# Performance work log

Hardware: AMD Instinct MI355X
Metric: run time of the kernel (lower is better)

The kernel has to match this reference:

```python
import jax, jax.numpy as jnp
import numpy as np

N_ATOMS, N_NBH, N_IN, N_FILTERS, N_OUT, N_GAUSS = 10000, 48, 128, 128, 128, 25
R_CUTOFF = 5.0
LOG2 = float(np.log(2.0))


def ssp(v):
    # shifted softplus, the SchNet activation
    return jax.nn.softplus(v) - LOG2


def setup_inputs() -> dict:
    key = jax.random.key(0)
    ks = jax.random.split(key, 10)
    x = jax.random.normal(ks[0], (N_ATOMS, N_IN), dtype=jnp.float32)
    dR = jax.random.uniform(ks[1], (N_ATOMS, N_NBH), dtype=jnp.float32) * 10.0  # distances in [0,10)
    dR_expanded = jax.random.normal(ks[2], (N_ATOMS, N_NBH, N_GAUSS), dtype=jnp.float32)
    pairwise_mask = jnp.ones((N_ATOMS, N_NBH), dtype=jnp.float32)
    neighbors_idx = jax.random.randint(ks[3], (N_ATOMS, N_NBH), 0, N_ATOMS, dtype=jnp.int32)
    s = 1.0 / np.sqrt(N_FILTERS)
    W1 = jax.random.normal(ks[4], (N_GAUSS, N_FILTERS), dtype=jnp.float32) * (1.0 / np.sqrt(N_GAUSS))
    b1 = jnp.zeros((N_FILTERS,), dtype=jnp.float32)
    W2 = jax.random.normal(ks[5], (N_FILTERS, N_FILTERS), dtype=jnp.float32) * s
    b2 = jnp.zeros((N_FILTERS,), dtype=jnp.float32)
    W_in2f = jax.random.normal(ks[6], (N_IN, N_FILTERS), dtype=jnp.float32) * (1.0 / np.sqrt(N_IN))
    W_f2out = jax.random.normal(ks[7], (N_FILTERS, N_OUT), dtype=jnp.float32) * s
    b_f2out = jnp.zeros((N_OUT,), dtype=jnp.float32)
    return {"x": x, "dR": dR, "dR_expanded": dR_expanded, "pairwise_mask": pairwise_mask,
            "neighbors_idx": neighbors_idx, "W1": W1, "b1": b1, "W2": W2, "b2": b2,
            "W_in2f": W_in2f, "W_f2out": W_f2out, "b_f2out": b_f2out}


def reference(x, dR, dR_expanded, pairwise_mask, neighbors_idx,
              W1, b1, W2, b2, W_in2f, W_f2out, b_f2out):
    # FilterNetwork: Dense + ssp + Dense, on Gaussian-smeared distances -> [N, K, F]
    W = jnp.einsum('nkg,gf->nkf', dR_expanded, W1) + b1
    W = jnp.einsum('nkf,fh->nkh', ssp(W), W2) + b2
    # HardCutoff: 1 where within cutoff
    C = (dR <= R_CUTOFF).astype(W.dtype)           # [N, K]
    W = W * C[..., None]
    # in2f (no bias), gather neighbor features
    y = x @ W_in2f                                  # [N, F]
    y = jnp.take(y, neighbors_idx, axis=0)          # [N, K, F] (gather == take_along_axis path)
    # filter-weighted multiply + masked sum aggregation over neighbor axis
    y = y * W
    y = jnp.sum(y * pairwise_mask[..., None], axis=1)  # [N, F]
    # f2out: Linear + shifted softplus
    return ssp(y @ W_f2out + b_f2out)               # [N, n_out]
```

## Files before the change

### kernel.cpp

```cpp
#include <hip/hip_runtime.h>
#include <hip/hip_bf16.h>


#define NA 10000
#define NK 48
#define NF 128
#define HP  136
#define YFP 136

typedef __bf16 bf16x8 __attribute__((ext_vector_type(8)));
typedef float  f32x4  __attribute__((ext_vector_type(4)));

__device__ __forceinline__ unsigned short f2bs(float x) {
    return __builtin_bit_cast(unsigned short, (__bf16)x);
}
__device__ __forceinline__ float bs2f(unsigned short u) {
    return (float)__builtin_bit_cast(__bf16, u);
}
__device__ __forceinline__ float sspf(float v) {
    return fmaxf(v, 0.0f) + __logf(1.0f + __expf(-fabsf(v))) - 0.69314718056f;
}

__global__ __launch_bounds__(256) void prep_weights(
    const float* __restrict__ W1,
    const float* __restrict__ W2,
    const float* __restrict__ Wi,
    const float* __restrict__ Wo,
    unsigned short* __restrict__ wsb)
{
    int i = blockIdx.x * 256 + threadIdx.x;
    if (i < 4096) {
        int f = i >> 5, g = i & 31;
        wsb[i] = (g < 25) ? f2bs(W1[g * NF + f]) : (unsigned short)0;
    } else if (i < 20480) {
        int j = i - 4096; int h = j >> 7, k = j & 127;
        wsb[i] = f2bs(W2[k * NF + h]);
    } else if (i < 36864) {
        int j = i - 20480; int f = j >> 7, k = j & 127;
        wsb[i] = f2bs(Wi[k * NF + f]);
    } else if (i < 53248) {
        int j = i - 36864; int f = j >> 7, k = j & 127;
        wsb[i] = f2bs(Wo[k * NF + f]);
    }
}

__global__ __launch_bounds__(256) void in2f_mfma(
    const float* __restrict__ x,
    const unsigned short* __restrict__ WiT,
    unsigned short* __restrict__ yfeatb)
{
    const int tid = threadIdx.x;
    const int w = tid >> 6;
    const int lane = tid & 63;
    const int r = lane & 15;
    const int q = lane >> 4;
    const int m0 = blockIdx.x * 64 + w * 16;
    const int row = m0 + r;
    const bool rv = (row < NA);

    f32x4 acc[8];
    #pragma unroll
    for (int nt = 0; nt < 8; ++nt) { acc[nt][0]=0.f; acc[nt][1]=0.f; acc[nt][2]=0.f; acc[nt][3]=0.f; }

    #pragma unroll
    for (int ks = 0; ks < 4; ++ks) {
        bf16x8 a;
        if (rv) {
            const float4* xp = (const float4*)(x + (size_t)row * NF + ks * 32 + q * 8);
            float4 v0 = xp[0], v1 = xp[1];
            a[0]=(__bf16)v0.x; a[1]=(__bf16)v0.y; a[2]=(__bf16)v0.z; a[3]=(__bf16)v0.w;
            a[4]=(__bf16)v1.x; a[5]=(__bf16)v1.y; a[6]=(__bf16)v1.z; a[7]=(__bf16)v1.w;
        } else {
            #pragma unroll
            for (int j = 0; j < 8; ++j) a[j] = (__bf16)0.0f;
        }
        #pragma unroll
        for (int nt = 0; nt < 8; ++nt) {
            bf16x8 b = *(const bf16x8*)(WiT + (nt * 16 + r) * NF + ks * 32 + q * 8);
            acc[nt] = __builtin_amdgcn_mfma_f32_16x16x32_bf16(a, b, acc[nt], 0, 0, 0);
        }
    }
    #pragma unroll
    for (int nt = 0; nt < 8; ++nt) {
        #pragma unroll
        for (int reg = 0; reg < 4; ++reg) {
            int orow = m0 + q * 4 + reg;
            if (orow < NA)
                yfeatb[(size_t)orow * NF + nt * 16 + r] = f2bs(acc[nt][reg]);
        }
    }
}

__global__ __launch_bounds__(256) void cfconv_mfma(
    const float* __restrict__ dR,
    const float* __restrict__ dRe,
    const float* __restrict__ mask,
    const int*   __restrict__ nbr,
    const float* __restrict__ b1,
    const float* __restrict__ b2,
    const unsigned short* __restrict__ W1T,
    const unsigned short* __restrict__ W2T,
    const unsigned short* __restrict__ yfeatb,
    float* __restrict__ yout)
{
    __shared__ __align__(16) unsigned short s_H[NK * HP];
    __shared__ __align__(16) unsigned short s_yf[NK * YFP];
    __shared__ float s_cm[NK];

    const int tid = threadIdx.x;
    const int n = blockIdx.x;
    const int w = tid >> 6;
    const int lane = tid & 63;
    const int r = lane & 15;
    const int q = lane >> 4;
    const int nt0 = w * 2;

    const int kb = tid >> 4;
    const int sp = tid & 15;
    const int nb0 = nbr[n * NK + kb] * NF;
    const int nb1 = nbr[n * NK + kb + 16] * NF;
    const int nb2 = nbr[n * NK + kb + 32] * NF;
    bf16x8 g0 = *(const bf16x8*)(yfeatb + nb0 + sp * 8);
    bf16x8 g1 = *(const bf16x8*)(yfeatb + nb1 + sp * 8);
    bf16x8 g2 = *(const bf16x8*)(yfeatb + nb2 + sp * 8);

    bf16x8 bfr0 = *(const bf16x8*)(W1T + ((nt0    ) * 16 + r) * 32 + q * 8);
    bf16x8 bfr1 = *(const bf16x8*)(W1T + ((nt0 + 1) * 16 + r) * 32 + q * 8);
    bf16x8 bw[2][4];
    #pragma unroll
    for (int t = 0; t < 2; ++t)
        #pragma unroll
        for (int ks = 0; ks < 4; ++ks)
            bw[t][ks] = *(const bf16x8*)(W2T + ((nt0 + t) * 16 + r) * NF + ks * 32 + q * 8);

    if (tid < NK) {
        float d = dR[n * NK + tid];
        float m = mask[n * NK + tid];
        s_cm[tid] = (d <= 5.0f) ? m : 0.0f;
    }

    const float bias1a = b1[nt0 * 16 + r];
    const float bias1b = b1[nt0 * 16 + 16 + r];
    const float bias2a = b2[nt0 * 16 + r];
    const float bias2b = b2[nt0 * 16 + 16 + r];

    const float* dre_n = dRe + (size_t)n * (NK * 25);
    #pragma unroll
    for (int mt = 0; mt < 3; ++mt) {
        bf16x8 a;
        if (q < 3) {
            float av[8];
            __builtin_memcpy(av, dre_n + (mt * 16 + r) * 25 + q * 8, 32);
            #pragma unroll
            for (int j = 0; j < 8; ++j) a[j] = (__bf16)av[j];
        } else {
            float v = dre_n[(mt * 16 + r) * 25 + 24];
            a[0] = (__bf16)v;
            #pragma unroll
            for (int j = 1; j < 8; ++j) a[j] = (__bf16)0.0f;
        }
        f32x4 zf; zf[0]=0.f; zf[1]=0.f; zf[2]=0.f; zf[3]=0.f;
        f32x4 h0v = __builtin_amdgcn_mfma_f32_16x16x32_bf16(a, bfr0, zf, 0, 0, 0);
        f32x4 h1v = __builtin_amdgcn_mfma_f32_16x16x32_bf16(a, bfr1, zf, 0, 0, 0);
        #pragma unroll
        for (int reg = 0; reg < 4; ++reg) {
            int k = mt * 16 + q * 4 + reg;
            s_H[k * HP + nt0 * 16 + r]      = f2bs(sspf(h0v[reg] + bias1a));
            s_H[k * HP + nt0 * 16 + 16 + r] = f2bs(sspf(h1v[reg] + bias1b));
        }
    }

    *(bf16x8*)(&s_yf[(kb     ) * YFP + sp * 8]) = g0;
    *(bf16x8*)(&s_yf[(kb + 16) * YFP + sp * 8]) = g1;
    *(bf16x8*)(&s_yf[(kb + 32) * YFP + sp * 8]) = g2;

    __syncthreads();

    f32x4 acc[3][2];
    #pragma unroll
    for (int mt = 0; mt < 3; ++mt)
        #pragma unroll
        for (int t = 0; t < 2; ++t) { acc[mt][t][0]=0.f; acc[mt][t][1]=0.f; acc[mt][t][2]=0.f; acc[mt][t][3]=0.f; }

    #pragma unroll
    for (int ks = 0; ks < 4; ++ks) {
        #pragma unroll
        for (int mt = 0; mt < 3; ++mt) {
            bf16x8 a = *(const bf16x8*)(&s_H[(mt * 16 + r) * HP + ks * 32 + q * 8]);
            acc[mt][0] = __builtin_amdgcn_mfma_f32_16x16x32_bf16(a, bw[0][ks], acc[mt][0], 0, 0, 0);
            acc[mt][1] = __builtin_amdgcn_mfma_f32_16x16x32_bf16(a, bw[1][ks], acc[mt][1], 0, 0, 0);
        }
    }

    float part0 = 0.f, part1 = 0.f;
    const int h0 = nt0 * 16 + r;
    #pragma unroll
    for (int mt = 0; mt < 3; ++mt) {
        #pragma unroll
        for (int reg = 0; reg < 4; ++reg) {
            int k = mt * 16 + q * 4 + reg;
            float cmk = s_cm[k];
            part0 += cmk * (acc[mt][0][reg] + bias2a) * bs2f(s_yf[k * YFP + h0]);
            part1 += cmk * (acc[mt][1][reg] + bias2b) * bs2f(s_yf[k * YFP + h0 + 16]);
        }
    }
    part0 += __shfl_xor(part0, 16);
    part0 += __shfl_xor(part0, 32);
    part1 += __shfl_xor(part1, 16);
    part1 += __shfl_xor(part1, 32);
    if (q == 0) {
        yout[(size_t)n * NF + h0]      = part0;
        yout[(size_t)n * NF + h0 + 16] = part1;
    }
}

__global__ __launch_bounds__(256) void f2out_mfma(
    const unsigned short* __restrict__ WoT,
    const float* __restrict__ bo,
    float* io)
{
    const int tid = threadIdx.x;
    const int w = tid >> 6;
    const int lane = tid & 63;
    const int r = lane & 15;
    const int q = lane >> 4;
    const int m0 = blockIdx.x * 64 + w * 16;
    const int row = m0 + r;
    const bool rv = (row < NA);

    f32x4 acc[8];
    #pragma unroll
    for (int nt = 0; nt < 8; ++nt) { acc[nt][0]=0.f; acc[nt][1]=0.f; acc[nt][2]=0.f; acc[nt][3]=0.f; }

    #pragma unroll
    for (int ks = 0; ks < 4; ++ks) {
        bf16x8 a;
        if (rv) {
            const float4* yp = (const float4*)(io + (size_t)row * NF + ks * 32 + q * 8);
            float4 v0 = yp[0], v1 = yp[1];
            a[0]=(__bf16)v0.x; a[1]=(__bf16)v0.y; a[2]=(__bf16)v0.z; a[3]=(__bf16)v0.w;
            a[4]=(__bf16)v1.x; a[5]=(__bf16)v1.y; a[6]=(__bf16)v1.z; a[7]=(__bf16)v1.w;
        } else {
            #pragma unroll
            for (int j = 0; j < 8; ++j) a[j] = (__bf16)0.0f;
        }
        #pragma unroll
        for (int nt = 0; nt < 8; ++nt) {
            bf16x8 b = *(const bf16x8*)(WoT + (nt * 16 + r) * NF + ks * 32 + q * 8);
            acc[nt] = __builtin_amdgcn_mfma_f32_16x16x32_bf16(a, b, acc[nt], 0, 0, 0);
        }
    }
    #pragma unroll
    for (int nt = 0; nt < 8; ++nt) {
        float bia = bo[nt * 16 + r];
        #pragma unroll
        for (int reg = 0; reg < 4; ++reg) {
            int orow = m0 + q * 4 + reg;
            if (orow < NA)
                io[(size_t)orow * NF + nt * 16 + r] = sspf(acc[nt][reg] + bia);
        }
    }
}

extern "C" void kernel_launch(void* const* d_in, const int* in_sizes, int n_in,
                              void* d_out, int out_size, void* d_ws, size_t ws_size,
                              hipStream_t stream)
{
    const float* x    = (const float*)d_in[0];
    const float* dR   = (const float*)d_in[1];
    const float* dRe  = (const float*)d_in[2];
    const float* mask = (const float*)d_in[3];
    const int*   nbr  = (const int*)d_in[4];
    const float* W1   = (const float*)d_in[5];
    const float* b1   = (const float*)d_in[6];
    const float* W2   = (const float*)d_in[7];
    const float* b2   = (const float*)d_in[8];
    const float* Wi2f = (const float*)d_in[9];
    const float* Wf2o = (const float*)d_in[10];
    const float* bf2o = (const float*)d_in[11];
    float* out = (float*)d_out;

    unsigned short* wsb = (unsigned short*)d_ws;
    unsigned short* W1T    = wsb;
    unsigned short* W2T    = wsb + 4096;
    unsigned short* WiT    = wsb + 20480;
    unsigned short* WoT    = wsb + 36864;
    unsigned short* yfeatb = wsb + 53248;

    prep_weights<<<208, 256, 0, stream>>>(W1, W2, Wi2f, Wf2o, wsb);
    in2f_mfma<<<157, 256, 0, stream>>>(x, WiT, yfeatb);
    cfconv_mfma<<<NA, 256, 0, stream>>>(dR, dRe, mask, nbr, b1, b2,
                                        W1T, W2T, yfeatb, out);
    f2out_mfma<<<157, 256, 0, stream>>>(WoT, bf2o, out);
}
```

Measured before the change: 198.4 us.

## Fuse f2out into cfconv and merge weight prep into in2f kernel

Merges the weight-prep and in2f kernels into one launch: extra blocks convert W1/W2/Wo to bf16, while the in2f blocks transpose Wi into shared memory themselves. The f2out linear plus shifted softplus is fused into the per-atom cfconv kernel, so each atom's aggregated features stay in shared memory and never make a round trip through global memory. The filter MFMA operands are swapped so the neighbor reduction becomes shuffles inside a 16-lane group. In exchange, each cfconv block runs a 1-row MFMA that wastes most of its 16 rows, and it adds a second barrier.

```diff
diff --git a/kernel.cpp b/kernel.cpp
--- a/kernel.cpp
+++ b/kernel.cpp
@@ -21,35 +21,49 @@
     return fmaxf(v, 0.0f) + __logf(1.0f + __expf(-fabsf(v))) - 0.69314718056f;
 }
 
-__global__ __launch_bounds__(256) void prep_weights(
+__global__ __launch_bounds__(256) void in2f_prep(
+    const float* __restrict__ x,
+    const float* __restrict__ Wi,
     const float* __restrict__ W1,
     const float* __restrict__ W2,
-    const float* __restrict__ Wi,
     const float* __restrict__ Wo,
-    unsigned short* __restrict__ wsb)
-{
-    int i = blockIdx.x * 256 + threadIdx.x;
-    if (i < 4096) {
-        int f = i >> 5, g = i & 31;
-        wsb[i] = (g < 25) ? f2bs(W1[g * NF + f]) : (unsigned short)0;
-    } else if (i < 20480) {
-        int j = i - 4096; int h = j >> 7, k = j & 127;
-        wsb[i] = f2bs(W2[k * NF + h]);
-    } else if (i < 36864) {
-        int j = i - 20480; int f = j >> 7, k = j & 127;
-        wsb[i] = f2bs(Wi[k * NF + f]);
-    } else if (i < 53248) {
-        int j = i - 36864; int f = j >> 7, k = j & 127;
-        wsb[i] = f2bs(Wo[k * NF + f]);
-    }
-}
-
-__global__ __launch_bounds__(256) void in2f_mfma(
-    const float* __restrict__ x,
-    const unsigned short* __restrict__ WiT,
+    unsigned short* __restrict__ wsb,
     unsigned short* __restrict__ yfeatb)
 {
     const int tid = threadIdx.x;
+
+    if (blockIdx.x >= 157) {
+        int i = (blockIdx.x - 157) * 256 + tid;
+        if (i < 4096) {
+            int f = i >> 5, g = i & 31;
+            wsb[i] = (g < 25) ? f2bs(W1[g * NF + f]) : (unsigned short)0;
+        } else if (i < 20480) {
+            int j = i - 4096; int h = j >> 7, k = j & 127;
+            wsb[i] = f2bs(W2[k * NF + h]);
+        } else {
+            int j = i - 20480; int f = j >> 7, k = j & 127;
+            wsb[i] = f2bs(Wo[k * NF + f]);
+        }
+        return;
+    }
+
+    __shared__ __align__(16) unsigned short s_wi[NF * 136];
+    {
+        const float4* wi4 = (const float4*)Wi;
+        #pragma unroll
+        for (int it = 0; it < 16; ++it) {
+            int idx4 = it * 256 + tid;
+            float4 v = wi4[idx4];
+            int i = idx4 >> 5;
+            int f = (idx4 & 31) * 4;
+            s_wi[(f + 0) * 136 + i] = f2bs(v.x);
+            s_wi[(f + 1) * 136 + i] = f2bs(v.y);
+            s_wi[(f + 2) * 136 + i] = f2bs(v.z);
+            s_wi[(f + 3) * 136 + i] = f2bs(v.w);
+        }
+    }
+    __syncthreads();
+
     const int w = tid >> 6;
     const int lane = tid & 63;
     const int r = lane & 15;
@@ -76,7 +90,7 @@
         }
         #pragma unroll
         for (int nt = 0; nt < 8; ++nt) {
-            bf16x8 b = *(const bf16x8*)(WiT + (nt * 16 + r) * NF + ks * 32 + q * 8);
+            bf16x8 b = *(const bf16x8*)(&s_wi[(nt * 16 + r) * 136 + ks * 32 + q * 8]);
             acc[nt] = __builtin_amdgcn_mfma_f32_16x16x32_bf16(a, b, acc[nt], 0, 0, 0);
         }
     }
@@ -98,13 +112,16 @@
     const int*   __restrict__ nbr,
     const float* __restrict__ b1,
     const float* __restrict__ b2,
+    const float* __restrict__ bf2o,
     const unsigned short* __restrict__ W1T,
     const unsigned short* __restrict__ W2T,
+    const unsigned short* __restrict__ WoT,
     const unsigned short* __restrict__ yfeatb,
-    float* __restrict__ yout)
+    float* __restrict__ out)
 {
     __shared__ __align__(16) unsigned short s_H[NK * HP];
     __shared__ __align__(16) unsigned short s_yf[NK * YFP];
+    __shared__ __align__(16) float s_y[NF];
     __shared__ float s_cm[NK];
 
     const int tid = threadIdx.x;
@@ -141,8 +158,6 @@
 
     const float bias1a = b1[nt0 * 16 + r];
     const float bias1b = b1[nt0 * 16 + 16 + r];
-    const float bias2a = b2[nt0 * 16 + r];
-    const float bias2b = b2[nt0 * 16 + 16 + r];
 
     const float* dre_n = dRe + (size_t)n * (NK * 25);
     #pragma unroll
@@ -176,88 +191,85 @@
 
     __syncthreads();
 
-    f32x4 acc[3][2];
-    #pragma unroll
-    for (int mt = 0; mt < 3; ++mt)
-        #pragma unroll
-        for (int t = 0; t < 2; ++t) { acc[mt][t][0]=0.f; acc[mt][t][1]=0.f; acc[mt][t][2]=0.f; acc[mt][t][3]=0.f; }
+    f32x4 acc[2][3];
+    #pragma unroll
+    for (int t = 0; t < 2; ++t)
+        #pragma unroll
+        for (int kt = 0; kt < 3; ++kt) { acc[t][kt][0]=0.f; acc[t][kt][1]=0.f; acc[t][kt][2]=0.f; acc[t][kt][3]=0.f; }
 
     #pragma unroll
     for (int ks = 0; ks < 4; ++ks) {
         #pragma unroll
-        for (int mt = 0; mt < 3; ++mt) {
-            bf16x8 a = *(const bf16x8*)(&s_H[(mt * 16 + r) * HP + ks * 32 + q * 8]);
-            acc[mt][0] = __builtin_amdgcn_mfma_f32_16x16x32_bf16(a, bw[0][ks], acc[mt][0], 0, 0, 0);
-            acc[mt][1] = __builtin_amdgcn_mfma_f32_16x16x32_bf16(a, bw[1][ks], acc[mt][1], 0, 0, 0);
-        }
-    }
-
-    float part0 = 0.f, part1 = 0.f;
-    const int h0 = nt0 * 16 + r;
-    #pragma unroll
-    for (int mt = 0; mt < 3; ++mt) {
+        for (int kt = 0; kt < 3; ++kt) {
+            bf16x8 bh = *(const bf16x8*)(&s_H[(kt * 16 + r) * HP + ks * 32 + q * 8]);
+            acc[0][kt] = __builtin_amdgcn_mfma_f32_16x16x32_bf16(bw[0][ks], bh, acc[0][kt], 0, 0, 0);
+            acc[1][kt] = __builtin_amdgcn_mfma_f32_16x16x32_bf16(bw[1][ks], bh, acc[1][kt], 0, 0, 0);
+        }
+    }
+
+    const float4 b2v0 = *(const float4*)(b2 + (nt0    ) * 16 + q * 4);
+    const float4 b2v1 = *(const float4*)(b2 + (nt0 + 1) * 16 + q * 4);
+    float cmv0 = s_cm[r], cmv1 = s_cm[16 + r], cmv2 = s_cm[32 + r];
+
+    float p0[4] = {0.f, 0.f, 0.f, 0.f};
+    float p1[4] = {0.f, 0.f, 0.f, 0.f};
+    #pragma unroll
+    for (int kt = 0; kt < 3; ++kt) {
+        float cmk = (kt == 0) ? cmv0 : (kt == 1) ? cmv1 : cmv2;
+        uint2 y0 = *(const uint2*)(&s_yf[(kt * 16 + r) * YFP + (nt0    ) * 16 + q * 4]);
+        uint2 y1 = *(const uint2*)(&s_yf[(kt * 16 + r) * YFP + (nt0 + 1) * 16 + q * 4]);
+        float yf0[4], yf1[4];
+        yf0[0] = __builtin_bit_cast(float, y0.x << 16);
+        yf0[1] = __builtin_bit_cast(float, y0.x & 0xffff0000u);
+        yf0[2] = __builtin_bit_cast(float, y0.y << 16);
+        yf0[3] = __builtin_bit_cast(float, y0.y & 0xffff0000u);
+        yf1[0] = __builtin_bit_cast(float, y1.x << 16);
+        yf1[1] = __builtin_bit_cast(float, y1.x & 0xffff0000u);
+        yf1[2] = __builtin_bit_cast(float, y1.y << 16);
+        yf1[3] = __builtin_bit_cast(float, y1.y & 0xffff0000u);
         #pragma unroll
         for (int reg = 0; reg < 4; ++reg) {
-            int k = mt * 16 + q * 4 + reg;
-            float cmk = s_cm[k];
-            part0 += cmk * (acc[mt][0][reg] + bias2a) * bs2f(s_yf[k * YFP + h0]);
-            part1 += cmk * (acc[mt][1][reg] + bias2b) * bs2f(s_yf[k * YFP + h0 + 16]);
-        }
-    }
-    part0 += __shfl_xor(part0, 16);
-    part0 += __shfl_xor(part0, 32);
-    part1 += __shfl_xor(part1, 16);
-    part1 += __shfl_xor(part1, 32);
-    if (q == 0) {
-        yout[(size_t)n * NF + h0]      = part0;
-        yout[(size_t)n * NF + h0 + 16] = part1;
-    }
-}
-
-__global__ __launch_bounds__(256) void f2out_mfma(
-    const unsigned short* __restrict__ WoT,
-    const float* __restrict__ bo,
-    float* io)
-{
-    const int tid = threadIdx.x;
-    const int w = tid >> 6;
-    const int lane = tid & 63;
-    const int r = lane & 15;
-    const int q = lane >> 4;
-    const int m0 = blockIdx.x * 64 + w * 16;
-    const int row = m0 + r;
-    const bool rv = (row < NA);
-
-    f32x4 acc[8];
-    #pragma unroll
-    for (int nt = 0; nt < 8; ++nt) { acc[nt][0]=0.f; acc[nt][1]=0.f; acc[nt][2]=0.f; acc[nt][3]=0.f; }
-
+            p0[reg] += cmk * ((acc[0][kt][reg] + b2v0[reg]) * yf0[reg]);
+            p1[reg] += cmk * ((acc[1][kt][reg] + b2v1[reg]) * yf1[reg]);
+        }
+    }
+    #pragma unroll
+    for (int m = 1; m <= 8; m <<= 1) {
+        #pragma unroll
+        for (int reg = 0; reg < 4; ++reg) {
+            p0[reg] += __shfl_xor(p0[reg], m);
+            p1[reg] += __shfl_xor(p1[reg], m);
+        }
+    }
+    if (r == 0) {
+        *(float4*)(&s_y[(nt0    ) * 16 + q * 4]) = float4{p0[0], p0[1], p0[2], p0[3]};
+        *(float4*)(&s_y[(nt0 + 1) * 16 + q * 4]) = float4{p1[0], p1[1], p1[2], p1[3]};
+    }
+    __syncthreads();
+
+    f32x4 acco0, acco1;
+    acco0[0]=0.f; acco0[1]=0.f; acco0[2]=0.f; acco0[3]=0.f;
+    acco1[0]=0.f; acco1[1]=0.f; acco1[2]=0.f; acco1[3]=0.f;
     #pragma unroll
     for (int ks = 0; ks < 4; ++ks) {
+        float4 ya = *(const float4*)(&s_y[ks * 32 + q * 8]);
+        float4 yb = *(const float4*)(&s_y[ks * 32 + q * 8 + 4]);
         bf16x8 a;
-        if (rv) {
-            const float4* yp = (const float4*)(io + (size_t)row * NF + ks * 32 + q * 8);
-            float4 v0 = yp[0], v1 = yp[1];
-            a[0]=(__bf16)v0.x; a[1]=(__bf16)v0.y; a[2]=(__bf16)v0.z; a[3]=(__bf16)v0.w;
-            a[4]=(__bf16)v1.x; a[5]=(__bf16)v1.y; a[6]=(__bf16)v1.z; a[7]=(__bf16)v1.w;
-        } else {
-            #pragma unroll
-            for (int j = 0; j < 8; ++j) a[j] = (__bf16)0.0f;
-        }
-        #pragma unroll
-        for (int nt = 0; nt < 8; ++nt) {
-            bf16x8 b = *(const bf16x8*)(WoT + (nt * 16 + r) * NF + ks * 32 + q * 8);
-            acc[nt] = __builtin_amdgcn_mfma_f32_16x16x32_bf16(a, b, acc[nt], 0, 0, 0);
-        }
-    }
-    #pragma unroll
-    for (int nt = 0; nt < 8; ++nt) {
-        float bia = bo[nt * 16 + r];
-        #pragma unroll
-        for (int reg = 0; reg < 4; ++reg) {
-            int orow = m0 + q * 4 + reg;
-            if (orow < NA)
-                io[(size_t)orow * NF + nt * 16 + r] = sspf(acc[nt][reg] + bia);
+        a[0]=(__bf16)ya.x; a[1]=(__bf16)ya.y; a[2]=(__bf16)ya.z; a[3]=(__bf16)ya.w;
+        a[4]=(__bf16)yb.x; a[5]=(__bf16)yb.y; a[6]=(__bf16)yb.z; a[7]=(__bf16)yb.w;
+        bf16x8 bo0 = *(const bf16x8*)(WoT + ((nt0    ) * 16 + r) * NF + ks * 32 + q * 8);
+        bf16x8 bo1 = *(const bf16x8*)(WoT + ((nt0 + 1) * 16 + r) * NF + ks * 32 + q * 8);
+        acco0 = __builtin_amdgcn_mfma_f32_16x16x32_bf16(a, bo0, acco0, 0, 0, 0);
+        acco1 = __builtin_amdgcn_mfma_f32_16x16x32_bf16(a, bo1, acco1, 0, 0, 0);
+    }
+    {
+        int f0 = nt0 * 16 + r;
+        int f1 = f0 + 16;
+        float o0 = sspf(acco0[0] + bf2o[f0]);
+        float o1 = sspf(acco1[0] + bf2o[f1]);
+        if (q == 0) {
+            out[(size_t)n * NF + f0] = o0;
+            out[(size_t)n * NF + f1] = o1;
         }
     }
 }
@@ -283,13 +295,10 @@
     unsigned short* wsb = (unsigned short*)d_ws;
     unsigned short* W1T    = wsb;
     unsigned short* W2T    = wsb + 4096;
-    unsigned short* WiT    = wsb + 20480;
-    unsigned short* WoT    = wsb + 36864;
-    unsigned short* yfeatb = wsb + 53248;
-
-    prep_weights<<<208, 256, 0, stream>>>(W1, W2, Wi2f, Wf2o, wsb);
-    in2f_mfma<<<157, 256, 0, stream>>>(x, WiT, yfeatb);
-    cfconv_mfma<<<NA, 256, 0, stream>>>(dR, dRe, mask, nbr, b1, b2,
-                                        W1T, W2T, yfeatb, out);
-    f2out_mfma<<<157, 256, 0, stream>>>(WoT, bf2o, out);
-}
+    unsigned short* WoT    = wsb + 20480;
+    unsigned short* yfeatb = wsb + 36864;
+
+    in2f_prep<<<301, 256, 0, stream>>>(x, Wi2f, W1, W2, Wf2o, wsb, yfeatb);
+    cfconv_mfma<<<NA, 256, 0, stream>>>(dR, dRe, mask, nbr, b1, b2, bf2o,
+                                        W1T, W2T, WoT, yfeatb, out);
+}
```

New measurement: 222.2 us. 12.0% more time.

## Fuse weight prep into in2f kernel and process two atoms per cfconv block

Applied to the files above, without the earlier changes.

Merges the weight-prep kernel into the in2f kernel: extra blocks convert W1/W2/Wo to bf16, and each in2f block transposes W_in2f into shared memory itself instead of reading a prepped copy. This removes one kernel launch and the dependency between prep and in2f. The cfconv kernel now handles two atoms per 512-thread block, halving the block count and doubling shared memory per block. The in2f blocks redo the Wi transpose redundantly, and cfconv occupancy may change with the larger shared footprint.

```diff
diff --git a/kernel.cpp b/kernel.cpp
--- a/kernel.cpp
+++ b/kernel.cpp
@@ -21,35 +21,49 @@
     return fmaxf(v, 0.0f) + __logf(1.0f + __expf(-fabsf(v))) - 0.69314718056f;
 }
 
-__global__ __launch_bounds__(256) void prep_weights(
+__global__ __launch_bounds__(256) void in2f_prep(
+    const float* __restrict__ x,
+    const float* __restrict__ Wi,
     const float* __restrict__ W1,
     const float* __restrict__ W2,
-    const float* __restrict__ Wi,
     const float* __restrict__ Wo,
-    unsigned short* __restrict__ wsb)
-{
-    int i = blockIdx.x * 256 + threadIdx.x;
-    if (i < 4096) {
-        int f = i >> 5, g = i & 31;
-        wsb[i] = (g < 25) ? f2bs(W1[g * NF + f]) : (unsigned short)0;
-    } else if (i < 20480) {
-        int j = i - 4096; int h = j >> 7, k = j & 127;
-        wsb[i] = f2bs(W2[k * NF + h]);
-    } else if (i < 36864) {
-        int j = i - 20480; int f = j >> 7, k = j & 127;
-        wsb[i] = f2bs(Wi[k * NF + f]);
-    } else if (i < 53248) {
-        int j = i - 36864; int f = j >> 7, k = j & 127;
-        wsb[i] = f2bs(Wo[k * NF + f]);
-    }
-}
-
-__global__ __launch_bounds__(256) void in2f_mfma(
-    const float* __restrict__ x,
-    const unsigned short* __restrict__ WiT,
+    unsigned short* __restrict__ wsb,
     unsigned short* __restrict__ yfeatb)
 {
     const int tid = threadIdx.x;
+
+    if (blockIdx.x >= 157) {
+        int i = (blockIdx.x - 157) * 256 + tid;
+        if (i < 4096) {
+            int f = i >> 5, g = i & 31;
+            wsb[i] = (g < 25) ? f2bs(W1[g * NF + f]) : (unsigned short)0;
+        } else if (i < 20480) {
+            int j = i - 4096; int h = j >> 7, k = j & 127;
+            wsb[i] = f2bs(W2[k * NF + h]);
+        } else {
+            int j = i - 20480; int f = j >> 7, k = j & 127;
+            wsb[i] = f2bs(Wo[k * NF + f]);
+        }
+        return;
+    }
+
+    __shared__ __align__(16) unsigned short s_wi[NF * 136];
+    {
+        const float4* wi4 = (const float4*)Wi;
+        #pragma unroll
+        for (int it = 0; it < 16; ++it) {
+            int idx4 = it * 256 + tid;
+            float4 v = wi4[idx4];
+            int i = idx4 >> 5;
+            int f = (idx4 & 31) * 4;
+            s_wi[(f + 0) * 136 + i] = f2bs(v.x);
+            s_wi[(f + 1) * 136 + i] = f2bs(v.y);
+            s_wi[(f + 2) * 136 + i] = f2bs(v.z);
+            s_wi[(f + 3) * 136 + i] = f2bs(v.w);
+        }
+    }
+    __syncthreads();
+
     const int w = tid >> 6;
     const int lane = tid & 63;
     const int r = lane & 15;
@@ -76,7 +90,7 @@
         }
         #pragma unroll
         for (int nt = 0; nt < 8; ++nt) {
-            bf16x8 b = *(const bf16x8*)(WiT + (nt * 16 + r) * NF + ks * 32 + q * 8);
+            bf16x8 b = *(const bf16x8*)(&s_wi[(nt * 16 + r) * 136 + ks * 32 + q * 8]);
             acc[nt] = __builtin_amdgcn_mfma_f32_16x16x32_bf16(a, b, acc[nt], 0, 0, 0);
         }
     }
@@ -91,7 +105,7 @@
     }
 }
 
-__global__ __launch_bounds__(256) void cfconv_mfma(
+__global__ __launch_bounds__(512) void cfconv_mfma(
     const float* __restrict__ dR,
     const float* __restrict__ dRe,
     const float* __restrict__ mask,
@@ -103,20 +117,22 @@
     const unsigned short* __restrict__ yfeatb,
     float* __restrict__ yout)
 {
-    __shared__ __align__(16) unsigned short s_H[NK * HP];
-    __shared__ __align__(16) unsigned short s_yf[NK * YFP];
-    __shared__ float s_cm[NK];
+    __shared__ __align__(16) unsigned short s_H[2][NK * HP];
+    __shared__ __align__(16) unsigned short s_yf[2][NK * YFP];
+    __shared__ float s_cm[2][NK];
 
     const int tid = threadIdx.x;
-    const int n = blockIdx.x;
-    const int w = tid >> 6;
+    const int a = tid >> 8;
+    const int t8 = tid & 255;
+    const int n = blockIdx.x * 2 + a;
+    const int w = t8 >> 6;
     const int lane = tid & 63;
     const int r = lane & 15;
     const int q = lane >> 4;
     const int nt0 = w * 2;
 
-    const int kb = tid >> 4;
-    const int sp = tid & 15;
+    const int kb = t8 >> 4;
+    const int sp = t8 & 15;
     const int nb0 = nbr[n * NK + kb] * NF;
     const int nb1 = nbr[n * NK + kb + 16] * NF;
     const int nb2 = nbr[n * NK + kb + 32] * NF;
@@ -133,10 +149,10 @@
         for (int ks = 0; ks < 4; ++ks)
             bw[t][ks] = *(const bf16x8*)(W2T + ((nt0 + t) * 16 + r) * NF + ks * 32 + q * 8);
 
-    if (tid < NK) {
-        float d = dR[n * NK + tid];
-        float m = mask[n * NK + tid];
-        s_cm[tid] = (d <= 5.0f) ? m : 0.0f;
+    if (t8 < NK) {
+        float d = dR[n * NK + t8];
+        float m = mask[n * NK + t8];
+        s_cm[a][t8] = (d <= 5.0f) ? m : 0.0f;
     }
 
     const float bias1a = b1[nt0 * 16 + r];
@@ -147,32 +163,32 @@
     const float* dre_n = dRe + (size_t)n * (NK * 25);
     #pragma unroll
     for (int mt = 0; mt < 3; ++mt) {
-        bf16x8 a;
+        bf16x8 av8;
         if (q < 3) {
             float av[8];
             __builtin_memcpy(av, dre_n + (mt * 16 + r) * 25 + q * 8, 32);
             #pragma unroll
-            for (int j = 0; j < 8; ++j) a[j] = (__bf16)av[j];
+            for (int j = 0; j < 8; ++j) av8[j] = (__bf16)av[j];
         } else {
             float v = dre_n[(mt * 16 + r) * 25 + 24];
-            a[0] = (__bf16)v;
+            av8[0] = (__bf16)v;
             #pragma unroll
-            for (int j = 1; j < 8; ++j) a[j] = (__bf16)0.0f;
+            for (int j = 1; j < 8; ++j) av8[j] = (__bf16)0.0f;
         }
         f32x4 zf; zf[0]=0.f; zf[1]=0.f; zf[2]=0.f; zf[3]=0.f;
-        f32x4 h0v = __builtin_amdgcn_mfma_f32_16x16x32_bf16(a, bfr0, zf, 0, 0, 0);
-        f32x4 h1v = __builtin_amdgcn_mfma_f32_16x16x32_bf16(a, bfr1, zf, 0, 0, 0);
+        f32x4 h0v = __builtin_amdgcn_mfma_f32_16x16x32_bf16(av8, bfr0, zf, 0, 0, 0);
+        f32x4 h1v = __builtin_amdgcn_mfma_f32_16x16x32_bf16(av8, bfr1, zf, 0, 0, 0);
         #pragma unroll
         for (int reg = 0; reg < 4; ++reg) {
             int k = mt * 16 + q * 4 + reg;
-            s_H[k * HP + nt0 * 16 + r]      = f2bs(sspf(h0v[reg] + bias1a));
-            s_H[k * HP + nt0 * 16 + 16 + r] = f2bs(sspf(h1v[reg] + bias1b));
-        }
-    }
-
-    *(bf16x8*)(&s_yf[(kb     ) * YFP + sp * 8]) = g0;
-    *(bf16x8*)(&s_yf[(kb + 16) * YFP + sp * 8]) = g1;
-    *(bf16x8*)(&s_yf[(kb + 32) * YFP + sp * 8]) = g2;
+            s_H[a][k * HP + nt0 * 16 + r]      = f2bs(sspf(h0v[reg] + bias1a));
+            s_H[a][k * HP + nt0 * 16 + 16 + r] = f2bs(sspf(h1v[reg] + bias1b));
+        }
+    }
+
+    *(bf16x8*)(&s_yf[a][(kb     ) * YFP + sp * 8]) = g0;
+    *(bf16x8*)(&s_yf[a][(kb + 16) * YFP + sp * 8]) = g1;
+    *(bf16x8*)(&s_yf[a][(kb + 32) * YFP + sp * 8]) = g2;
 
     __syncthreads();
 
@@ -186,9 +202,9 @@
     for (int ks = 0; ks < 4; ++ks) {
         #pragma unroll
         for (int mt = 0; mt < 3; ++mt) {
-            bf16x8 a = *(const bf16x8*)(&s_H[(mt * 16 + r) * HP + ks * 32 + q * 8]);
-            acc[mt][0] = __builtin_amdgcn_mfma_f32_16x16x32_bf16(a, bw[0][ks], acc[mt][0], 0, 0, 0);
-            acc[mt][1] = __builtin_amdgcn_mfma_f32_16x16x32_bf16(a, bw[1][ks], acc[mt][1], 0, 0, 0);
+            bf16x8 ah = *(const bf16x8*)(&s_H[a][(mt * 16 + r) * HP + ks * 32 + q * 8]);
+            acc[mt][0] = __builtin_amdgcn_mfma_f32_16x16x32_bf16(ah, bw[0][ks], acc[mt][0], 0, 0, 0);
+            acc[mt][1] = __builtin_amdgcn_mfma_f32_16x16x32_bf16(ah, bw[1][ks], acc[mt][1], 0, 0, 0);
         }
     }
 
@@ -199,9 +215,9 @@
         #pragma unroll
         for (int reg = 0; reg < 4; ++reg) {
             int k = mt * 16 + q * 4 + reg;
-            float cmk = s_cm[k];
-            part0 += cmk * (acc[mt][0][reg] + bias2a) * bs2f(s_yf[k * YFP + h0]);
-            part1 += cmk * (acc[mt][1][reg] + bias2b) * bs2f(s_yf[k * YFP + h0 + 16]);
+            float cmk = s_cm[a][k];
+            part0 += cmk * (acc[mt][0][reg] + bias2a) * bs2f(s_yf[a][k * YFP + h0]);
+            part1 += cmk * (acc[mt][1][reg] + bias2b) * bs2f(s_yf[a][k * YFP + h0 + 16]);
         }
     }
     part0 += __shfl_xor(part0, 16);
@@ -283,13 +299,11 @@
     unsigned short* wsb = (unsigned short*)d_ws;
     unsigned short* W1T    = wsb;
     unsigned short* W2T    = wsb + 4096;
-    unsigned short* WiT    = wsb + 20480;
-    unsigned short* WoT    = wsb + 36864;
-    unsigned short* yfeatb = wsb + 53248;
-
-    prep_weights<<<208, 256, 0, stream>>>(W1, W2, Wi2f, Wf2o, wsb);
-    in2f_mfma<<<157, 256, 0, stream>>>(x, WiT, yfeatb);
-    cfconv_mfma<<<NA, 256, 0, stream>>>(dR, dRe, mask, nbr, b1, b2,
-                                        W1T, W2T, yfeatb, out);
+    unsigned short* WoT    = wsb + 20480;
+    unsigned short* yfeatb = wsb + 36864;
+
+    in2f_prep<<<301, 256, 0, stream>>>(x, Wi2f, W1, W2, Wf2o, wsb, yfeatb);
+    cfconv_mfma<<<NA / 2, 512, 0, stream>>>(dR, dRe, mask, nbr, b1, b2,
+                                            W1T, W2T, yfeatb, out);
     f2out_mfma<<<157, 256, 0, stream>>>(WoT, bf2o, out);
 }
```

After: 211.2 us. 6.4% more time.

## Halve cfconv block to 128 threads, each wave covering four filter tiles

Applied to the files above, without the earlier changes.

The per-atom cfconv block drops from 4 waves to 2, so each wave handles four 16-wide filter tiles. The second filter GEMM and the reduction run in two passes, and each thread gathers six neighbor rows instead of three. The aim is to lower per-block overhead, fit more blocks per CU, and reuse the staged H tile across more output columns per wave. In exchange each wave does twice the serial work, and the loads of W2 into registers now sit after the barrier, which may leave less latency hidden per block.

```diff
diff --git a/kernel.cpp b/kernel.cpp
--- a/kernel.cpp
+++ b/kernel.cpp
@@ -91,7 +91,7 @@
     }
 }
 
-__global__ __launch_bounds__(256) void cfconv_mfma(
+__global__ __launch_bounds__(128, 3) void cfconv_d(
     const float* __restrict__ dR,
     const float* __restrict__ dRe,
     const float* __restrict__ mask,
@@ -113,25 +113,21 @@
     const int lane = tid & 63;
     const int r = lane & 15;
     const int q = lane >> 4;
-    const int nt0 = w * 2;
+    const int ft0 = w * 4;
 
     const int kb = tid >> 4;
     const int sp = tid & 15;
-    const int nb0 = nbr[n * NK + kb] * NF;
-    const int nb1 = nbr[n * NK + kb + 16] * NF;
-    const int nb2 = nbr[n * NK + kb + 32] * NF;
-    bf16x8 g0 = *(const bf16x8*)(yfeatb + nb0 + sp * 8);
-    bf16x8 g1 = *(const bf16x8*)(yfeatb + nb1 + sp * 8);
-    bf16x8 g2 = *(const bf16x8*)(yfeatb + nb2 + sp * 8);
-
-    bf16x8 bfr0 = *(const bf16x8*)(W1T + ((nt0    ) * 16 + r) * 32 + q * 8);
-    bf16x8 bfr1 = *(const bf16x8*)(W1T + ((nt0 + 1) * 16 + r) * 32 + q * 8);
-    bf16x8 bw[2][4];
-    #pragma unroll
-    for (int t = 0; t < 2; ++t)
-        #pragma unroll
-        for (int ks = 0; ks < 4; ++ks)
-            bw[t][ks] = *(const bf16x8*)(W2T + ((nt0 + t) * 16 + r) * NF + ks * 32 + q * 8);
+    bf16x8 g[6];
+    #pragma unroll
+    for (int j = 0; j < 6; ++j) {
+        int base = nbr[n * NK + kb + 8 * j] * NF;
+        g[j] = *(const bf16x8*)(yfeatb + base + sp * 8);
+    }
+
+    bf16x8 bfr[4];
+    #pragma unroll
+    for (int t = 0; t < 4; ++t)
+        bfr[t] = *(const bf16x8*)(W1T + ((ft0 + t) * 16 + r) * 32 + q * 8);
 
     if (tid < NK) {
         float d = dR[n * NK + tid];
@@ -139,78 +135,92 @@
         s_cm[tid] = (d <= 5.0f) ? m : 0.0f;
     }
 
-    const float bias1a = b1[nt0 * 16 + r];
-    const float bias1b = b1[nt0 * 16 + 16 + r];
-    const float bias2a = b2[nt0 * 16 + r];
-    const float bias2b = b2[nt0 * 16 + 16 + r];
+    float bias1[4];
+    #pragma unroll
+    for (int t = 0; t < 4; ++t) bias1[t] = b1[(ft0 + t) * 16 + r];
 
     const float* dre_n = dRe + (size_t)n * (NK * 25);
     #pragma unroll
     for (int mt = 0; mt < 3; ++mt) {
-        bf16x8 a;
+        bf16x8 av8;
         if (q < 3) {
             float av[8];
             __builtin_memcpy(av, dre_n + (mt * 16 + r) * 25 + q * 8, 32);
             #pragma unroll
-            for (int j = 0; j < 8; ++j) a[j] = (__bf16)av[j];
+            for (int j = 0; j < 8; ++j) av8[j] = (__bf16)av[j];
         } else {
             float v = dre_n[(mt * 16 + r) * 25 + 24];
-            a[0] = (__bf16)v;
-            #pragma unroll
-            for (int j = 1; j < 8; ++j) a[j] = (__bf16)0.0f;
-        }
-        f32x4 zf; zf[0]=0.f; zf[1]=0.f; zf[2]=0.f; zf[3]=0.f;
-        f32x4 h0v = __builtin_amdgcn_mfma_f32_16x16x32_bf16(a, bfr0, zf, 0, 0, 0);
-        f32x4 h1v = __builtin_amdgcn_mfma_f32_16x16x32_bf16(a, bfr1, zf, 0, 0, 0);
-        #pragma unroll
-        for (int reg = 0; reg < 4; ++reg) {
-            int k = mt * 16 + q * 4 + reg;
-            s_H[k * HP + nt0 * 16 + r]      = f2bs(sspf(h0v[reg] + bias1a));
-            s_H[k * HP + nt0 * 16 + 16 + r] = f2bs(sspf(h1v[reg] + bias1b));
-        }
-    }
-
-    *(bf16x8*)(&s_yf[(kb     ) * YFP + sp * 8]) = g0;
-    *(bf16x8*)(&s_yf[(kb + 16) * YFP + sp * 8]) = g1;
-    *(bf16x8*)(&s_yf[(kb + 32) * YFP + sp * 8]) = g2;
+            av8[0] = (__bf16)v;
+            #pragma unroll
+            for (int j = 1; j < 8; ++j) av8[j] = (__bf16)0.0f;
+        }
+        #pragma unroll
+        for (int t = 0; t < 4; ++t) {
+            f32x4 zf; zf[0]=0.f; zf[1]=0.f; zf[2]=0.f; zf[3]=0.f;
+            f32x4 h = __builtin_amdgcn_mfma_f32_16x16x32_bf16(av8, bfr[t], zf, 0, 0, 0);
+            #pragma unroll
+            for (int reg = 0; reg < 4; ++reg) {
+                int k = mt * 16 + q * 4 + reg;
+                s_H[k * HP + (ft0 + t) * 16 + r] = f2bs(sspf(h[reg] + bias1[t]));
+            }
+        }
+    }
+
+    #pragma unroll
+    for (int j = 0; j < 6; ++j)
+        *(bf16x8*)(&s_yf[(kb + 8 * j) * YFP + sp * 8]) = g[j];
 
     __syncthreads();
 
-    f32x4 acc[3][2];
-    #pragma unroll
-    for (int mt = 0; mt < 3; ++mt)
-        #pragma unroll
-        for (int t = 0; t < 2; ++t) { acc[mt][t][0]=0.f; acc[mt][t][1]=0.f; acc[mt][t][2]=0.f; acc[mt][t][3]=0.f; }
-
-    #pragma unroll
-    for (int ks = 0; ks < 4; ++ks) {
+    #pragma unroll
+    for (int p = 0; p < 2; ++p) {
+        const int nt0 = ft0 + 2 * p;
+
+        bf16x8 bw[2][4];
+        #pragma unroll
+        for (int t = 0; t < 2; ++t)
+            #pragma unroll
+            for (int ks = 0; ks < 4; ++ks)
+                bw[t][ks] = *(const bf16x8*)(W2T + ((nt0 + t) * 16 + r) * NF + ks * 32 + q * 8);
+        const float bias2a = b2[nt0 * 16 + r];
+        const float bias2b = b2[nt0 * 16 + 16 + r];
+
+        f32x4 acc[3][2];
+        #pragma unroll
+        for (int mt = 0; mt < 3; ++mt)
+            #pragma unroll
+            for (int t = 0; t < 2; ++t) { acc[mt][t][0]=0.f; acc[mt][t][1]=0.f; acc[mt][t][2]=0.f; acc[mt][t][3]=0.f; }
+
+        #pragma unroll
+        for (int ks = 0; ks < 4; ++ks) {
+            #pragma unroll
+            for (int mt = 0; mt < 3; ++mt) {
+                bf16x8 ah = *(const bf16x8*)(&s_H[(mt * 16 + r) * HP + ks * 32 + q * 8]);
+                acc[mt][0] = __builtin_amdgcn_mfma_f32_16x16x32_bf16(ah, bw[0][ks], acc[mt][0], 0, 0, 0);
+                acc[mt][1] = __builtin_amdgcn_mfma_f32_16x16x32_bf16(ah, bw[1][ks], acc[mt][1], 0, 0, 0);
+            }
+        }
+
+        float part0 = 0.f, part1 = 0.f;
+        const int h0 = nt0 * 16 + r;
         #pragma unroll
         for (int mt = 0; mt < 3; ++mt) {
-            bf16x8 a = *(const bf16x8*)(&s_H[(mt * 16 + r) * HP + ks * 32 + q * 8]);
-            acc[mt][0] = __builtin_amdgcn_mfma_f32_16x16x32_bf16(a, bw[0][ks], acc[mt][0], 0, 0, 0);
-            acc[mt][1] = __builtin_amdgcn_mfma_f32_16x16x32_bf16(a, bw[1][ks], acc[mt][1], 0, 0, 0);
-        }
-    }
-
-    float part0 = 0.f, part1 = 0.f;
-    const int h0 = nt0 * 16 + r;
-    #pragma unroll
-    for (int mt = 0; mt < 3; ++mt) {
-        #pragma unroll
-        for (int reg = 0; reg < 4; ++reg) {
-            int k = mt * 16 + q * 4 + reg;
-            float cmk = s_cm[k];
-            part0 += cmk * (acc[mt][0][reg] + bias2a) * bs2f(s_yf[k * YFP + h0]);
-            part1 += cmk * (acc[mt][1][reg] + bias2b) * bs2f(s_yf[k * YFP + h0 + 16]);
-        }
-    }
-    part0 += __shfl_xor(part0, 16);
-    part0 += __shfl_xor(part0, 32);
-    part1 += __shfl_xor(part1, 16);
-    part1 += __shfl_xor(part1, 32);
-    if (q == 0) {
-        yout[(size_t)n * NF + h0]      = part0;
-        yout[(size_t)n * NF + h0 + 16] = part1;
+            #pragma unroll
+            for (int reg = 0; reg < 4; ++reg) {
+                int k = mt * 16 + q * 4 + reg;
+                float cmk = s_cm[k];
+                part0 += cmk * (acc[mt][0][reg] + bias2a) * bs2f(s_yf[k * YFP + h0]);
+                part1 += cmk * (acc[mt][1][reg] + bias2b) * bs2f(s_yf[k * YFP + h0 + 16]);
+            }
+        }
+        part0 += __shfl_xor(part0, 16);
+        part0 += __shfl_xor(part0, 32);
+        part1 += __shfl_xor(part1, 16);
+        part1 += __shfl_xor(part1, 32);
+        if (q == 0) {
+            yout[(size_t)n * NF + h0]      = part0;
+            yout[(size_t)n * NF + h0 + 16] = part1;
+        }
     }
 }
 
@@ -289,7 +299,7 @@
 
     prep_weights<<<208, 256, 0, stream>>>(W1, W2, Wi2f, Wf2o, wsb);
     in2f_mfma<<<157, 256, 0, stream>>>(x, WiT, yfeatb);
-    cfconv_mfma<<<NA, 256, 0, stream>>>(dR, dRe, mask, nbr, b1, b2,
-                                        W1T, W2T, yfeatb, out);
+    cfconv_d<<<NA, 128, 0, stream>>>(dR, dRe, mask, nbr, b1, b2,
+                                     W1T, W2T, yfeatb, out);
     f2out_mfma<<<157, 256, 0, stream>>>(WoT, bf2o, out);
 }
```

Result: no change. 197.2 us (-0.6%).
